# Performance work log

Hardware: AMD Instinct MI355X
Metric: run time of the kernel (lower is better)

The kernel has to match this reference:

```python
import jax, jax.numpy as jnp
import numpy as np

# fatigue class -> emotion target distribution; row 3 is the uniform fallback
_TABLE = np.array([
    [0.05, 0.02, 0.03, 0.4, 0.05, 0.4, 0.05],
    [0.05, 0.05, 0.05, 0.05, 0.3, 0.05, 0.45],
    [0.1, 0.15, 0.2, 0.02, 0.35, 0.03, 0.15],
    [1.0 / 7.0] * 7,
], dtype=np.float32)

B = 4_000_000

def setup_inputs() -> dict:
    key = jax.random.key(0)
    k1, k2, k3 = jax.random.split(key, 3)
    fatigue_logits = jax.random.normal(k1, (B, 3), dtype=jnp.float32)
    emotion_logits = jax.random.normal(k2, (B, 7), dtype=jnp.float32)
    fatigue_targets = jax.random.randint(k3, (B,), 0, 4, dtype=jnp.int64)
    return {"fatigue_logits": fatigue_logits,
            "emotion_logits": emotion_logits,
            "fatigue_targets": fatigue_targets}

def reference(fatigue_logits, emotion_logits, fatigue_targets):
    eps = 1e-8
    table = jnp.asarray(_TABLE)
    # targets outside {0,1,2} map to the uniform row (index 3)
    idx = jnp.where((fatigue_targets >= 0) & (fatigue_targets <= 2), fatigue_targets, 3)
    target = table[idx]                      # [B, 7] gather from tiny LUT
    target = target + eps
    target = target / jnp.sum(target, axis=-1, keepdims=True)
    probs = jax.nn.softmax(emotion_logits, axis=-1)
    log_input = jnp.log(probs + eps)
    # F.kl_div(log_input, target, reduction='batchmean')
    kl = jnp.sum(target * (jnp.log(target) - log_input)) / target.shape[0]
    return kl
```

## Files before the change

kernel.cpp:

```cpp
#include <hip/hip_runtime.h>
#include <cmath>

struct KLC {
    float w0[7], w1[7], w2[7], w3[7];
    float cst0, cst1, cst2, cst3;
};

__device__ __forceinline__ float row_kl(const float* __restrict__ x, int t, const KLC& kc) {
    int c = ((unsigned)t <= 2u) ? t : 3;

    float m = x[0];
    #pragma unroll
    for (int j = 1; j < 7; ++j) m = fmaxf(m, x[j]);

    float Z = 0.0f;
    #pragma unroll
    for (int j = 0; j < 7; ++j) Z += __expf(x[j] - m);

    float d0 = 0.f, d1 = 0.f, d2 = 0.f, d3 = 0.f;
    #pragma unroll
    for (int j = 0; j < 7; ++j) {
        d0 = fmaf(kc.w0[j], x[j], d0);
        d1 = fmaf(kc.w1[j], x[j], d1);
        d2 = fmaf(kc.w2[j], x[j], d2);
        d3 = fmaf(kc.w3[j], x[j], d3);
    }
    float dw = (c == 0) ? d0 : (c == 1) ? d1 : (c == 2) ? d2 : d3;
    float cs = (c == 0) ? kc.cst0 : (c == 1) ? kc.cst1 : (c == 2) ? kc.cst2 : kc.cst3;

    return cs - dw + m + __logf(Z);
}

__global__ __launch_bounds__(256) void kl_main(
    const float* __restrict__ logits,
    const int*   __restrict__ tgt,
    long long nquad, int rem,
    double* __restrict__ partial,
    KLC kc)
{
    const float4* __restrict__ lg4 = (const float4*)logits;
    const int4*   __restrict__ tg4 = (const int4*)tgt;

    long long gid    = (long long)blockIdx.x * blockDim.x + threadIdx.x;
    long long stride = (long long)gridDim.x * blockDim.x;

    float local = 0.0f;
    for (long long q = gid; q < nquad; q += stride) {
        float4 f0 = lg4[q * 7 + 0];
        float4 f1 = lg4[q * 7 + 1];
        float4 f2 = lg4[q * 7 + 2];
        float4 f3 = lg4[q * 7 + 3];
        float4 f4 = lg4[q * 7 + 4];
        float4 f5 = lg4[q * 7 + 5];
        float4 f6 = lg4[q * 7 + 6];
        int4   tq = tg4[q];

        float v[28] = { f0.x, f0.y, f0.z, f0.w,
                        f1.x, f1.y, f1.z, f1.w,
                        f2.x, f2.y, f2.z, f2.w,
                        f3.x, f3.y, f3.z, f3.w,
                        f4.x, f4.y, f4.z, f4.w,
                        f5.x, f5.y, f5.z, f5.w,
                        f6.x, f6.y, f6.z, f6.w };
        int tt[4] = { tq.x, tq.y, tq.z, tq.w };

        #pragma unroll
        for (int r = 0; r < 4; ++r)
            local += row_kl(&v[r * 7], tt[r], kc);
    }

    if (blockIdx.x == 0 && threadIdx.x == 0) {
        for (int r = 0; r < rem; ++r) {
            long long row = nquad * 4 + r;
            float x[7];
            #pragma unroll
            for (int j = 0; j < 7; ++j) x[j] = logits[row * 7 + j];
            local += row_kl(x, tgt[row], kc);
        }
    }

    #pragma unroll
    for (int off = 32; off > 0; off >>= 1)
        local += __shfl_down(local, off, 64);

    __shared__ float smem[4];
    int lane = threadIdx.x & 63;
    int wid  = threadIdx.x >> 6;
    if (lane == 0) smem[wid] = local;
    __syncthreads();
    if (threadIdx.x == 0)
        partial[blockIdx.x] = (double)(smem[0] + smem[1] + smem[2] + smem[3]);
}

__global__ __launch_bounds__(256) void kl_reduce(
    const double* __restrict__ partial, int nb,
    float* __restrict__ out, int B)
{
    double s = 0.0;
    for (int i = threadIdx.x; i < nb; i += 256) s += partial[i];

    #pragma unroll
    for (int off = 32; off > 0; off >>= 1)
        s += __shfl_down(s, off, 64);

    __shared__ double smem[4];
    int lane = threadIdx.x & 63;
    int wid  = threadIdx.x >> 6;
    if (lane == 0) smem[wid] = s;
    __syncthreads();
    if (threadIdx.x == 0)
        out[0] = (float)((smem[0] + smem[1] + smem[2] + smem[3]) / (double)B);
}

extern "C" void kernel_launch(void* const* d_in, const int* in_sizes, int n_in,
                              void* d_out, int out_size, void* d_ws, size_t ws_size,
                              hipStream_t stream) {
    const float* emotion = (const float*)d_in[1];
    const int*   targets = (const int*)d_in[2];
    float*  out     = (float*)d_out;
    double* partial = (double*)d_ws;

    const int B = in_sizes[2];
    const long long nquad = B / 4;
    const int rem = B & 3;

    int nb = 1024;
    if ((size_t)nb * sizeof(double) > ws_size)
        nb = (int)(ws_size / sizeof(double));

    static const double T[4][7] = {
        {0.05, 0.02, 0.03, 0.4, 0.05, 0.4, 0.05},
        {0.05, 0.05, 0.05, 0.05, 0.3, 0.05, 0.45},
        {0.1, 0.15, 0.2, 0.02, 0.35, 0.03, 0.15},
        {1.0/7.0, 1.0/7.0, 1.0/7.0, 1.0/7.0, 1.0/7.0, 1.0/7.0, 1.0/7.0},
    };
    const double eps = 1e-8;
    KLC kc;
    float* wrows[4] = { kc.w0, kc.w1, kc.w2, kc.w3 };
    float* csts[4]  = { &kc.cst0, &kc.cst1, &kc.cst2, &kc.cst3 };
    for (int c = 0; c < 4; ++c) {
        double s = 0.0;
        for (int j = 0; j < 7; ++j) s += T[c][j] + eps;
        double cst = 0.0;
        for (int j = 0; j < 7; ++j) {
            double w = (T[c][j] + eps) / s;
            wrows[c][j] = (float)w;
            cst += w * std::log(w);
        }
        *csts[c] = (float)cst;
    }

    kl_main<<<nb, 256, 0, stream>>>(emotion, targets, nquad, rem, partial, kc);
    kl_reduce<<<1, 256, 0, stream>>>(partial, nb, out, B);
}
```

Before: 197.1 us.

## Stage logits through LDS for coalesced loads and move tail to reduce kernel

The main kernel now processes 1024-row chunks per block. Each thread loads float4s with consecutive-thread addresses, so global reads are fully coalesced. The data is then transposed through a 28 KB shared-memory buffer so each thread still gets 4 whole rows. This replaces the previous stride-7 float4 pattern per thread, which hit memory less efficiently. The leftover rows are handled in parallel by the reduce kernel. The cost is two block barriers per chunk, LDS bank traffic on the strided reads, and lower occupancy from the shared buffer.

```diff
diff --git a/kernel.cpp b/kernel.cpp
--- a/kernel.cpp
+++ b/kernel.cpp
@@ -34,49 +34,42 @@
 __global__ __launch_bounds__(256) void kl_main(
     const float* __restrict__ logits,
     const int*   __restrict__ tgt,
-    long long nquad, int rem,
+    int nchunks,
     double* __restrict__ partial,
     KLC kc)
 {
+    __shared__ float lds[7168];
+    float4* lds4 = (float4*)lds;
     const float4* __restrict__ lg4 = (const float4*)logits;
     const int4*   __restrict__ tg4 = (const int4*)tgt;
 
-    long long gid    = (long long)blockIdx.x * blockDim.x + threadIdx.x;
-    long long stride = (long long)gridDim.x * blockDim.x;
+    const int t = threadIdx.x;
+    float local = 0.0f;
 
-    float local = 0.0f;
-    for (long long q = gid; q < nquad; q += stride) {
-        float4 f0 = lg4[q * 7 + 0];
-        float4 f1 = lg4[q * 7 + 1];
-        float4 f2 = lg4[q * 7 + 2];
-        float4 f3 = lg4[q * 7 + 3];
-        float4 f4 = lg4[q * 7 + 4];
-        float4 f5 = lg4[q * 7 + 5];
-        float4 f6 = lg4[q * 7 + 6];
-        int4   tq = tg4[q];
+    for (int ch = blockIdx.x; ch < nchunks; ch += gridDim.x) {
+        const long long base4 = (long long)ch * 1792;
 
-        float v[28] = { f0.x, f0.y, f0.z, f0.w,
-                        f1.x, f1.y, f1.z, f1.w,
-                        f2.x, f2.y, f2.z, f2.w,
-                        f3.x, f3.y, f3.z, f3.w,
-                        f4.x, f4.y, f4.z, f4.w,
-                        f5.x, f5.y, f5.z, f5.w,
-                        f6.x, f6.y, f6.z, f6.w };
+        float4 r[7];
+        #pragma unroll
+        for (int k = 0; k < 7; ++k) r[k] = lg4[base4 + k * 256 + t];
+        int4 tq = tg4[(long long)ch * 256 + t];
+
+        __syncthreads();
+        #pragma unroll
+        for (int k = 0; k < 7; ++k) lds4[k * 256 + t] = r[k];
+        __syncthreads();
+
+        float v[28];
+        #pragma unroll
+        for (int k = 0; k < 7; ++k) {
+            float4 c = lds4[t * 7 + k];
+            v[4 * k + 0] = c.x; v[4 * k + 1] = c.y;
+            v[4 * k + 2] = c.z; v[4 * k + 3] = c.w;
+        }
         int tt[4] = { tq.x, tq.y, tq.z, tq.w };
-
         #pragma unroll
-        for (int r = 0; r < 4; ++r)
-            local += row_kl(&v[r * 7], tt[r], kc);
-    }
-
-    if (blockIdx.x == 0 && threadIdx.x == 0) {
-        for (int r = 0; r < rem; ++r) {
-            long long row = nquad * 4 + r;
-            float x[7];
-            #pragma unroll
-            for (int j = 0; j < 7; ++j) x[j] = logits[row * 7 + j];
-            local += row_kl(x, tgt[row], kc);
-        }
+        for (int rr = 0; rr < 4; ++rr)
+            local += row_kl(&v[rr * 7], tt[rr], kc);
     }
 
     #pragma unroll
@@ -93,11 +86,24 @@
 }
 
 __global__ __launch_bounds__(256) void kl_reduce(
+    const float* __restrict__ logits,
+    const int*   __restrict__ tgt,
+    long long tail_start, int tail,
     const double* __restrict__ partial, int nb,
-    float* __restrict__ out, int B)
+    float* __restrict__ out, int B, KLC kc)
 {
     double s = 0.0;
     for (int i = threadIdx.x; i < nb; i += 256) s += partial[i];
+
+    float tl = 0.0f;
+    for (int r = threadIdx.x; r < tail; r += 256) {
+        long long row = tail_start + r;
+        float x[7];
+        #pragma unroll
+        for (int j = 0; j < 7; ++j) x[j] = logits[row * 7 + j];
+        tl += row_kl(x, tgt[row], kc);
+    }
+    s += (double)tl;
 
     #pragma unroll
     for (int off = 32; off > 0; off >>= 1)
@@ -121,10 +127,12 @@
     double* partial = (double*)d_ws;
 
     const int B = in_sizes[2];
-    const long long nquad = B / 4;
-    const int rem = B & 3;
+    const int nchunks = B / 1024;
+    const int tail = B - nchunks * 1024;
+    const long long tail_start = (long long)nchunks * 1024;
 
     int nb = 1024;
+    if (nb > nchunks && nchunks > 0) nb = nchunks;
     if ((size_t)nb * sizeof(double) > ws_size)
         nb = (int)(ws_size / sizeof(double));
 
@@ -150,6 +158,7 @@
         *csts[c] = (float)cst;
     }
 
-    kl_main<<<nb, 256, 0, stream>>>(emotion, targets, nquad, rem, partial, kc);
-    kl_reduce<<<1, 256, 0, stream>>>(partial, nb, out, B);
+    kl_main<<<nb, 256, 0, stream>>>(emotion, targets, nchunks, partial, kc);
+    kl_reduce<<<1, 256, 0, stream>>>(emotion, targets, tail_start, tail,
+                                     partial, nb, out, B, kc);
 }
```

New measurement: 220.3 us. +11.8%, slower.
